# Kernel optimization log

Measured on AMD Instinct MI355X. Metric: run time of the kernel, lower is better.

Reference implementation:

```python
import itertools
import jax, jax.numpy as jnp
import numpy as np

# --- static configuration (matches init_kwargs) ---
B, O, V = 16, 24, 2            # batch, num_objects, num_total_variables
P0, P1, P2 = 32, 64, 64        # nullary/unary/binary predicate widths
R, C = 3, 16                   # len(arities)=3 ([0,1,2]), num_conjuncts
UI, BI = 1, 2                  # unary_index, binary_index in sorted arities [0,1,2]
NUM_IN = P0 + V * P1 + V * (V - 1) * P2  # 288

# permutation index tables (precomputed constants, as in build())
PERM_IDXS = np.array(list(itertools.permutations(range(O), V)))  # [P, V]
P = PERM_IDXS.shape[0]  # O*(O-1) = 552
_bin_idxs = np.stack(np.nonzero(1 - np.eye(V))).T.reshape(V, V - 1, 2)
_perm_bidxs = PERM_IDXS[:, _bin_idxs]                       # [P, V, V-1, 2]
_shift = (_perm_bidxs[..., 1] > _perm_bidxs[..., 0]).astype(int)
PERM_BIDXS = np.stack([_perm_bidxs[..., 0], _perm_bidxs[..., 1] - _shift], -1)  # [P,V,V-1,2]
BI0 = jnp.asarray(PERM_BIDXS[..., 0])
BI1 = jnp.asarray(PERM_BIDXS[..., 1])


def _probsum(x, axis):
    """Probabilistic OR reduction: 1 - prod(1 - x)."""
    return 1.0 - jnp.prod(1.0 - x, axis=axis)


def setup_inputs() -> dict:
    key = jax.random.key(0)
    k0, k1, k2, k3, k4 = jax.random.split(key, 5)
    return {
        "nullary": jax.random.uniform(k0, (B, P0), dtype=jnp.float32),
        "unary": jax.random.uniform(k1, (B, O, P1), dtype=jnp.float32),
        "binary": jax.random.uniform(k2, (B, O, O - 1, P2), dtype=jnp.float32),
        "and_kernel": 1.0 + 0.1 * jax.random.normal(k3, (R, C, NUM_IN, 3), dtype=jnp.float32),
        "or_kernel": 1.0 + 0.1 * jax.random.normal(k4, (R, C), dtype=jnp.float32),
        "temperature": jnp.ones((), dtype=jnp.float32),
    }


def reference(nullary, unary, binary, and_kernel, or_kernel, temperature):
    # --- compute_permutations ---
    perm_nullary = jnp.broadcast_to(nullary[:, None], (B, P, P0))       # [B,P,P0]
    perm_unary = unary[:, PERM_IDXS]                                    # [B,P,V,P1]
    perm_binary = binary[:, BI0, BI1]                                   # [B,P,V,V-1,P2]
    in_tensor = jnp.concatenate(
        [perm_nullary, perm_unary.reshape(B, P, -1), perm_binary.reshape(B, P, -1)], -1
    )  # [B, P, NUM_IN]

    # --- conjunct (AND) evaluation ---
    ak = jax.nn.softmax(and_kernel / temperature, axis=-1)              # [R,C,NUM_IN,3]
    x = in_tensor[:, :, None, None]                                     # [B,P,1,1,NUM_IN]
    conj_eval = x * ak[..., 0] + (1.0 - x) * ak[..., 1] + ak[..., 2]    # [B,P,R,C,NUM_IN]
    conjuncts = jnp.prod(conj_eval, axis=-1)                            # [B,P,R,C]

    # --- per-arity permutation reductions (OR over unbound variables) ---
    nullary_rules = _probsum(conjuncts[..., :UI, :], axis=1)            # [B,UI,C]
    unary_rules = conjuncts[..., UI:BI, :].reshape(B, O, P // O, BI - UI, C)
    unary_rules = _probsum(unary_rules, axis=2)                         # [B,O,BI-UI,C]
    binary_rules = conjuncts[..., BI:, :].reshape(
        B, O, O - 1, P // (O * (O - 1)), R - BI, C
    )
    binary_rules = _probsum(binary_rules, axis=3)                       # [B,O,O-1,R-BI,C]

    # --- disjunction (OR) over conjuncts ---
    ok = jax.nn.sigmoid(or_kernel / temperature)                        # [R,C]
    nullary_out = _probsum(nullary_rules * ok[:UI], -1)                 # [B,UI]
    unary_out = _probsum(unary_rules * ok[UI:BI], -1)                   # [B,O,BI-UI]
    binary_out = _probsum(binary_rules * ok[BI:], -1)                   # [B,O,O-1,R-BI]
    return nullary_out, unary_out, binary_out
```

## Files before the change

kernel.cpp:

```cpp
#include <hip/hip_runtime.h>
#include <math.h>


__device__ __forceinline__ float sigm(float x) { return 1.0f / (1.0f + expf(-x)); }

__global__ __launch_bounds__(256) void prep_kernel(const float* __restrict__ ak,
                                                   const float* __restrict__ temp,
                                                   float* __restrict__ dke) {
    int idx = blockIdx.x * 256 + threadIdx.x;
    if (idx >= 3 * 16 * 288) return;
    int i = idx % 288;
    int c = (idx / 288) % 16;
    int r = idx / (16 * 288);
    float invT = 1.0f / temp[0];
    const float* p = ak + (size_t)idx * 3;
    float a0 = p[0] * invT, a1 = p[1] * invT, a2 = p[2] * invT;
    float mx = fmaxf(a0, fmaxf(a1, a2));
    float e0 = expf(a0 - mx), e1 = expf(a1 - mx), e2 = expf(a2 - mx);
    float inv = 1.0f / (e0 + e1 + e2);
    float s0 = e0 * inv, s1 = e1 * inv, s2 = e2 * inv;
    int ch = i >> 2, lane = i & 3;
    float* q = dke + (((size_t)(ch * 16 + c) * 3 + r) * 8) + lane;
    q[0] = s0 - s1;
    q[4] = s1 + s2;
}

__global__ __launch_bounds__(256) void conj_part(const float* __restrict__ nullary,
                                                 const float* __restrict__ unary,
                                                 const float* __restrict__ binary,
                                                 const float* __restrict__ dke,
                                                 float* __restrict__ ws1) {
    __shared__ float xs[24 * 148];
    __shared__ float part[4][64][18];

    const int tid = threadIdx.x;
    const int blk = blockIdx.x;
    const int b = blk / 48;
    const int rem = blk % 48;
    const int a = rem >> 1;
    const int q = rem & 1;
    const int chbase = q * 36;

    for (int idx = tid; idx < 24 * 36; idx += 256) {
        int perm = idx / 36;
        int lc = idx % 36;
        int gc = chbase + lc;
        int je = perm < 23 ? perm : 22;
        int bb = je + (je >= a ? 1 : 0);
        int aadj = (a > bb) ? (a - 1) : a;
        const float* src;
        if (gc < 8)        src = nullary + b * 32 + gc * 4;
        else if (gc < 24)  src = unary + ((size_t)b * 24 + a) * 64 + (gc - 8) * 4;
        else if (gc < 40)  src = unary + ((size_t)b * 24 + bb) * 64 + (gc - 24) * 4;
        else if (gc < 56)  src = binary + (((size_t)b * 24 + a) * 23 + je) * 64 + (gc - 40) * 4;
        else               src = binary + (((size_t)b * 24 + bb) * 23 + aadj) * 64 + (gc - 56) * 4;
        float4 v = *(const float4*)src;
        *(float4*)&xs[perm * 148 + lc * 4] = v;
    }
    __syncthreads();

    const int iq = tid >> 6;
    const int pl = (tid >> 4) & 3;
    const int c  = tid & 15;

    float acc[6][3];
#pragma unroll
    for (int m = 0; m < 6; ++m)
#pragma unroll
        for (int r = 0; r < 3; ++r) acc[m][r] = 1.0f;

    const int lc0 = iq * 9;
#pragma unroll 3
    for (int lc = lc0; lc < lc0 + 9; ++lc) {
        float4 xv[6];
#pragma unroll
        for (int m = 0; m < 6; ++m)
            xv[m] = *(const float4*)&xs[(pl + 4 * m) * 148 + lc * 4];
        const float* kp = dke + (size_t)((chbase + lc) * 16 + c) * 24;
#pragma unroll
        for (int r = 0; r < 3; ++r) {
            float4 d = *(const float4*)(kp + r * 8);
            float4 e = *(const float4*)(kp + r * 8 + 4);
#pragma unroll
            for (int m = 0; m < 6; ++m) {
                float t0 = fmaf(xv[m].x, d.x, e.x);
                float t1 = fmaf(xv[m].y, d.y, e.y);
                float t2 = fmaf(xv[m].z, d.z, e.z);
                float t3 = fmaf(xv[m].w, d.w, e.w);
                acc[m][r] *= (t0 * t1) * (t2 * t3);
            }
        }
    }

    {
        float* p = part[iq][pl * 16 + c];
#pragma unroll
        for (int m = 0; m < 6; ++m)
#pragma unroll
            for (int r = 0; r < 3; ++r) p[m * 3 + r] = acc[m][r];
    }
    __syncthreads();

    if (iq == 0) {
        const int row = pl * 16 + c;
        float* dst = ws1 + (size_t)blk * 18 * 64;
#pragma unroll
        for (int m = 0; m < 6; ++m)
#pragma unroll
            for (int r = 0; r < 3; ++r)
                dst[(m * 3 + r) * 64 + row] =
                    part[0][row][m * 3 + r] * part[1][row][m * 3 + r]
                  * part[2][row][m * 3 + r] * part[3][row][m * 3 + r];
    }
}

__global__ __launch_bounds__(64) void combine_kernel(const float* __restrict__ ws1,
                                                     const float* __restrict__ orK,
                                                     const float* __restrict__ temp,
                                                     float* __restrict__ out,
                                                     float* __restrict__ ws0) {
    const int tid = threadIdx.x;
    const int b = blockIdx.x / 24;
    const int a = blockIdx.x % 24;
    const int pl = tid >> 4;
    const int c = tid & 15;

    const float* s0p = ws1 + ((size_t)(b * 48 + a * 2 + 0) * 18) * 64;
    const float* s1p = ws1 + ((size_t)(b * 48 + a * 2 + 1) * 18) * 64;

    float acc[6][3];
#pragma unroll
    for (int m = 0; m < 6; ++m)
#pragma unroll
        for (int r = 0; r < 3; ++r)
            acc[m][r] = s0p[(m * 3 + r) * 64 + tid] * s1p[(m * 3 + r) * 64 + tid];

    const float T = temp[0];
    const float ok2 = sigm(orK[32 + c] / T);

#pragma unroll
    for (int m = 0; m < 6; ++m) {
        int j = pl + 4 * m;
        float w = 1.0f - acc[m][2] * ok2;
#pragma unroll
        for (int off = 1; off < 16; off <<= 1) w *= __shfl_xor(w, off, 16);
        if (c == 0 && j < 23) out[400 + ((size_t)b * 24 + a) * 23 + j] = 1.0f - w;
    }

    float u1 = 1.0f, u0 = 1.0f;
#pragma unroll
    for (int m = 0; m < 6; ++m) {
        int j = pl + 4 * m;
        if (j < 23) {
            u1 *= (1.0f - acc[m][1]);
            u0 *= (1.0f - acc[m][0]);
        }
    }
    u1 *= __shfl_xor(u1, 16, 64);  u1 *= __shfl_xor(u1, 32, 64);
    u0 *= __shfl_xor(u0, 16, 64);  u0 *= __shfl_xor(u0, 32, 64);

    {
        float ok1 = sigm(orK[16 + c] / T);
        float w = 1.0f - (1.0f - u1) * ok1;
#pragma unroll
        for (int off = 1; off < 16; off <<= 1) w *= __shfl_xor(w, off, 16);
        if (tid == 0) out[16 + (size_t)b * 24 + a] = 1.0f - w;
    }
    if (pl == 0) ws0[((size_t)b * 24 + a) * 16 + c] = u0;
}

__global__ __launch_bounds__(256) void final_kernel(const float* __restrict__ ws0,
                                                    const float* __restrict__ orK,
                                                    const float* __restrict__ temp,
                                                    float* __restrict__ out) {
    int tid = threadIdx.x;
    int b = tid >> 4, c = tid & 15;
    float p = 1.0f;
#pragma unroll
    for (int a = 0; a < 24; ++a) p *= ws0[((size_t)b * 24 + a) * 16 + c];
    float T = temp[0];
    float ok0 = sigm(orK[c] / T);
    float w = 1.0f - (1.0f - p) * ok0;
#pragma unroll
    for (int off = 1; off < 16; off <<= 1) w *= __shfl_xor(w, off, 16);
    if (c == 0) out[b] = 1.0f - w;
}

extern "C" void kernel_launch(void* const* d_in, const int* in_sizes, int n_in,
                              void* d_out, int out_size, void* d_ws, size_t ws_size,
                              hipStream_t stream) {
    const float* nullary = (const float*)d_in[0];
    const float* unary   = (const float*)d_in[1];
    const float* binary  = (const float*)d_in[2];
    const float* ak      = (const float*)d_in[3];
    const float* orK     = (const float*)d_in[4];
    const float* temp    = (const float*)d_in[5];

    float* out = (float*)d_out;
    float* dke = (float*)d_ws;
    float* ws0 = dke + 27648;
    float* ws1 = ws0 + 6144;

    prep_kernel<<<54, 256, 0, stream>>>(ak, temp, dke);
    conj_part<<<768, 256, 0, stream>>>(nullary, unary, binary, dke, ws1);
    combine_kernel<<<384, 64, 0, stream>>>(ws1, orK, temp, out, ws0);
    final_kernel<<<1, 256, 0, stream>>>(ws0, orK, temp, out);
}
```

Measured before the change: 85.90 us.

## Fuse conjunct and combine kernels into one 512-thread block per (b,a)

```diff
diff --git a/kernel.cpp b/kernel.cpp
--- a/kernel.cpp
+++ b/kernel.cpp
@@ -1,6 +1,8 @@
 #include <hip/hip_runtime.h>
 #include <math.h>
 
+
+#define XST 290
 
 __device__ __forceinline__ float sigm(float x) { return 1.0f / (1.0f + expf(-x)); }
 
@@ -25,26 +27,24 @@
     q[4] = s1 + s2;
 }
 
-__global__ __launch_bounds__(256) void conj_part(const float* __restrict__ nullary,
-                                                 const float* __restrict__ unary,
-                                                 const float* __restrict__ binary,
-                                                 const float* __restrict__ dke,
-                                                 float* __restrict__ ws1) {
-    __shared__ float xs[24 * 148];
-    __shared__ float part[4][64][18];
+__global__ __launch_bounds__(512, 4) void mega_kernel(const float* __restrict__ nullary,
+                                                      const float* __restrict__ unary,
+                                                      const float* __restrict__ binary,
+                                                      const float* __restrict__ dke,
+                                                      const float* __restrict__ orK,
+                                                      const float* __restrict__ temp,
+                                                      float* __restrict__ out,
+                                                      float* __restrict__ ws0) {
+    __shared__ float xs[24 * XST];
+    __shared__ float part[7][64][18];
 
     const int tid = threadIdx.x;
-    const int blk = blockIdx.x;
-    const int b = blk / 48;
-    const int rem = blk % 48;
-    const int a = rem >> 1;
-    const int q = rem & 1;
-    const int chbase = q * 36;
-
-    for (int idx = tid; idx < 24 * 36; idx += 256) {
-        int perm = idx / 36;
-        int lc = idx % 36;
-        int gc = chbase + lc;
+    const int b = blockIdx.x / 24;
+    const int a = blockIdx.x % 24;
+
+    for (int idx = tid; idx < 24 * 72; idx += 512) {
+        int perm = idx / 72;
+        int gc = idx % 72;
         int je = perm < 23 ? perm : 22;
         int bb = je + (je >= a ? 1 : 0);
         int aadj = (a > bb) ? (a - 1) : a;
@@ -55,7 +55,7 @@
         else if (gc < 56)  src = binary + (((size_t)b * 24 + a) * 23 + je) * 64 + (gc - 40) * 4;
         else               src = binary + (((size_t)b * 24 + bb) * 23 + aadj) * 64 + (gc - 56) * 4;
         float4 v = *(const float4*)src;
-        *(float4*)&xs[perm * 148 + lc * 4] = v;
+        *(float4*)&xs[perm * XST + gc * 4] = v;
     }
     __syncthreads();
 
@@ -70,30 +70,67 @@
         for (int r = 0; r < 3; ++r) acc[m][r] = 1.0f;
 
     const int lc0 = iq * 9;
-#pragma unroll 3
-    for (int lc = lc0; lc < lc0 + 9; ++lc) {
+
+    float4 dcur[3], ecur[3];
+    {
+        const float* kp = dke + (size_t)(lc0 * 16 + c) * 24;
+#pragma unroll
+        for (int r = 0; r < 3; ++r) {
+            dcur[r] = *(const float4*)(kp + r * 8);
+            ecur[r] = *(const float4*)(kp + r * 8 + 4);
+        }
+    }
+
+#pragma unroll 2
+    for (int lc = lc0; lc < lc0 + 8; ++lc) {
+        float4 dnxt[3], enxt[3];
+        {
+            const float* kn = dke + (size_t)((lc + 1) * 16 + c) * 24;
+#pragma unroll
+            for (int r = 0; r < 3; ++r) {
+                dnxt[r] = *(const float4*)(kn + r * 8);
+                enxt[r] = *(const float4*)(kn + r * 8 + 4);
+            }
+        }
         float4 xv[6];
 #pragma unroll
         for (int m = 0; m < 6; ++m)
-            xv[m] = *(const float4*)&xs[(pl + 4 * m) * 148 + lc * 4];
-        const float* kp = dke + (size_t)((chbase + lc) * 16 + c) * 24;
+            xv[m] = *(const float4*)&xs[(pl + 4 * m) * XST + lc * 4];
 #pragma unroll
         for (int r = 0; r < 3; ++r) {
-            float4 d = *(const float4*)(kp + r * 8);
-            float4 e = *(const float4*)(kp + r * 8 + 4);
 #pragma unroll
             for (int m = 0; m < 6; ++m) {
-                float t0 = fmaf(xv[m].x, d.x, e.x);
-                float t1 = fmaf(xv[m].y, d.y, e.y);
-                float t2 = fmaf(xv[m].z, d.z, e.z);
-                float t3 = fmaf(xv[m].w, d.w, e.w);
+                float t0 = fmaf(xv[m].x, dcur[r].x, ecur[r].x);
+                float t1 = fmaf(xv[m].y, dcur[r].y, ecur[r].y);
+                float t2 = fmaf(xv[m].z, dcur[r].z, ecur[r].z);
+                float t3 = fmaf(xv[m].w, dcur[r].w, ecur[r].w);
                 acc[m][r] *= (t0 * t1) * (t2 * t3);
             }
         }
-    }
-
+#pragma unroll
+        for (int r = 0; r < 3; ++r) { dcur[r] = dnxt[r]; ecur[r] = enxt[r]; }
+    }
     {
-        float* p = part[iq][pl * 16 + c];
+        const int lc = lc0 + 8;
+        float4 xv[6];
+#pragma unroll
+        for (int m = 0; m < 6; ++m)
+            xv[m] = *(const float4*)&xs[(pl + 4 * m) * XST + lc * 4];
+#pragma unroll
+        for (int r = 0; r < 3; ++r) {
+#pragma unroll
+            for (int m = 0; m < 6; ++m) {
+                float t0 = fmaf(xv[m].x, dcur[r].x, ecur[r].x);
+                float t1 = fmaf(xv[m].y, dcur[r].y, ecur[r].y);
+                float t2 = fmaf(xv[m].z, dcur[r].z, ecur[r].z);
+                float t3 = fmaf(xv[m].w, dcur[r].w, ecur[r].w);
+                acc[m][r] *= (t0 * t1) * (t2 * t3);
+            }
+        }
+    }
+
+    if (iq >= 1) {
+        float* p = part[iq - 1][pl * 16 + c];
 #pragma unroll
         for (int m = 0; m < 6; ++m)
 #pragma unroll
@@ -103,70 +140,47 @@
 
     if (iq == 0) {
         const int row = pl * 16 + c;
-        float* dst = ws1 + (size_t)blk * 18 * 64;
-#pragma unroll
-        for (int m = 0; m < 6; ++m)
-#pragma unroll
-            for (int r = 0; r < 3; ++r)
-                dst[(m * 3 + r) * 64 + row] =
-                    part[0][row][m * 3 + r] * part[1][row][m * 3 + r]
-                  * part[2][row][m * 3 + r] * part[3][row][m * 3 + r];
-    }
-}
-
-__global__ __launch_bounds__(64) void combine_kernel(const float* __restrict__ ws1,
-                                                     const float* __restrict__ orK,
-                                                     const float* __restrict__ temp,
-                                                     float* __restrict__ out,
-                                                     float* __restrict__ ws0) {
-    const int tid = threadIdx.x;
-    const int b = blockIdx.x / 24;
-    const int a = blockIdx.x % 24;
-    const int pl = tid >> 4;
-    const int c = tid & 15;
-
-    const float* s0p = ws1 + ((size_t)(b * 48 + a * 2 + 0) * 18) * 64;
-    const float* s1p = ws1 + ((size_t)(b * 48 + a * 2 + 1) * 18) * 64;
-
-    float acc[6][3];
-#pragma unroll
-    for (int m = 0; m < 6; ++m)
-#pragma unroll
-        for (int r = 0; r < 3; ++r)
-            acc[m][r] = s0p[(m * 3 + r) * 64 + tid] * s1p[(m * 3 + r) * 64 + tid];
-
-    const float T = temp[0];
-    const float ok2 = sigm(orK[32 + c] / T);
-
-#pragma unroll
-    for (int m = 0; m < 6; ++m) {
-        int j = pl + 4 * m;
-        float w = 1.0f - acc[m][2] * ok2;
-#pragma unroll
-        for (int off = 1; off < 16; off <<= 1) w *= __shfl_xor(w, off, 16);
-        if (c == 0 && j < 23) out[400 + ((size_t)b * 24 + a) * 23 + j] = 1.0f - w;
-    }
-
-    float u1 = 1.0f, u0 = 1.0f;
-#pragma unroll
-    for (int m = 0; m < 6; ++m) {
-        int j = pl + 4 * m;
-        if (j < 23) {
-            u1 *= (1.0f - acc[m][1]);
-            u0 *= (1.0f - acc[m][0]);
-        }
-    }
-    u1 *= __shfl_xor(u1, 16, 64);  u1 *= __shfl_xor(u1, 32, 64);
-    u0 *= __shfl_xor(u0, 16, 64);  u0 *= __shfl_xor(u0, 32, 64);
-
-    {
-        float ok1 = sigm(orK[16 + c] / T);
-        float w = 1.0f - (1.0f - u1) * ok1;
-#pragma unroll
-        for (int off = 1; off < 16; off <<= 1) w *= __shfl_xor(w, off, 16);
-        if (tid == 0) out[16 + (size_t)b * 24 + a] = 1.0f - w;
-    }
-    if (pl == 0) ws0[((size_t)b * 24 + a) * 16 + c] = u0;
+#pragma unroll
+        for (int s = 0; s < 7; ++s)
+#pragma unroll
+            for (int m = 0; m < 6; ++m)
+#pragma unroll
+                for (int r = 0; r < 3; ++r)
+                    acc[m][r] *= part[s][row][m * 3 + r];
+
+        const float T = temp[0];
+        const float ok2 = sigm(orK[32 + c] / T);
+
+#pragma unroll
+        for (int m = 0; m < 6; ++m) {
+            int j = pl + 4 * m;
+            float w = 1.0f - acc[m][2] * ok2;
+#pragma unroll
+            for (int off = 1; off < 16; off <<= 1) w *= __shfl_xor(w, off, 16);
+            if (c == 0 && j < 23) out[400 + ((size_t)b * 24 + a) * 23 + j] = 1.0f - w;
+        }
+
+        float u1 = 1.0f, u0 = 1.0f;
+#pragma unroll
+        for (int m = 0; m < 6; ++m) {
+            int j = pl + 4 * m;
+            if (j < 23) {
+                u1 *= (1.0f - acc[m][1]);
+                u0 *= (1.0f - acc[m][0]);
+            }
+        }
+        u1 *= __shfl_xor(u1, 16, 64);  u1 *= __shfl_xor(u1, 32, 64);
+        u0 *= __shfl_xor(u0, 16, 64);  u0 *= __shfl_xor(u0, 32, 64);
+
+        {
+            float ok1 = sigm(orK[16 + c] / T);
+            float w = 1.0f - (1.0f - u1) * ok1;
+#pragma unroll
+            for (int off = 1; off < 16; off <<= 1) w *= __shfl_xor(w, off, 16);
+            if (tid == 0) out[16 + (size_t)b * 24 + a] = 1.0f - w;
+        }
+        if (pl == 0) ws0[((size_t)b * 24 + a) * 16 + c] = u0;
+    }
 }
 
 __global__ __launch_bounds__(256) void final_kernel(const float* __restrict__ ws0,
@@ -199,10 +213,8 @@
     float* out = (float*)d_out;
     float* dke = (float*)d_ws;
     float* ws0 = dke + 27648;
-    float* ws1 = ws0 + 6144;
 
     prep_kernel<<<54, 256, 0, stream>>>(ak, temp, dke);
-    conj_part<<<768, 256, 0, stream>>>(nullary, unary, binary, dke, ws1);
-    combine_kernel<<<384, 64, 0, stream>>>(ws1, orK, temp, out, ws0);
+    mega_kernel<<<16 * 24, 512, 0, stream>>>(nullary, unary, binary, dke, orK, temp, out, ws0);
     final_kernel<<<1, 256, 0, stream>>>(ws0, orK, temp, out);
 }
```

Measured after the change: 85.83 us. No clear change (-0.1%).

## Fuse conjunct evaluation and combine into one 1024-thread kernel per two objects

Applied to the files above, without the earlier changes.

```diff
diff --git a/kernel.cpp b/kernel.cpp
--- a/kernel.cpp
+++ b/kernel.cpp
@@ -1,6 +1,8 @@
 #include <hip/hip_runtime.h>
 #include <math.h>
 
+
+#define XST 290
 
 __device__ __forceinline__ float sigm(float x) { return 1.0f / (1.0f + expf(-x)); }
 
@@ -25,26 +27,26 @@
     q[4] = s1 + s2;
 }
 
-__global__ __launch_bounds__(256) void conj_part(const float* __restrict__ nullary,
-                                                 const float* __restrict__ unary,
-                                                 const float* __restrict__ binary,
-                                                 const float* __restrict__ dke,
-                                                 float* __restrict__ ws1) {
-    __shared__ float xs[24 * 148];
-    __shared__ float part[4][64][18];
+__global__ __launch_bounds__(1024, 4) void mega_kernel(const float* __restrict__ nullary,
+                                                       const float* __restrict__ unary,
+                                                       const float* __restrict__ binary,
+                                                       const float* __restrict__ dke,
+                                                       const float* __restrict__ orK,
+                                                       const float* __restrict__ temp,
+                                                       float* __restrict__ out,
+                                                       float* __restrict__ ws0) {
+    __shared__ float xs[2][24 * XST];
+    __shared__ float part[2][7][64][18];
 
     const int tid = threadIdx.x;
-    const int blk = blockIdx.x;
-    const int b = blk / 48;
-    const int rem = blk % 48;
-    const int a = rem >> 1;
-    const int q = rem & 1;
-    const int chbase = q * 36;
+    const int half = tid >> 9;
+    const int t9 = tid & 511;
+    const int b = blockIdx.x / 12;
+    const int a = (blockIdx.x % 12) * 2 + half;
 
-    for (int idx = tid; idx < 24 * 36; idx += 256) {
-        int perm = idx / 36;
-        int lc = idx % 36;
-        int gc = chbase + lc;
+    for (int idx = t9; idx < 24 * 72; idx += 512) {
+        int perm = idx / 72;
+        int gc = idx % 72;
         int je = perm < 23 ? perm : 22;
         int bb = je + (je >= a ? 1 : 0);
         int aadj = (a > bb) ? (a - 1) : a;
@@ -55,13 +57,13 @@
         else if (gc < 56)  src = binary + (((size_t)b * 24 + a) * 23 + je) * 64 + (gc - 40) * 4;
         else               src = binary + (((size_t)b * 24 + bb) * 23 + aadj) * 64 + (gc - 56) * 4;
         float4 v = *(const float4*)src;
-        *(float4*)&xs[perm * 148 + lc * 4] = v;
+        *(float4*)&xs[half][perm * XST + gc * 4] = v;
     }
     __syncthreads();
 
-    const int iq = tid >> 6;
-    const int pl = (tid >> 4) & 3;
-    const int c  = tid & 15;
+    const int iq = t9 >> 6;
+    const int pl = (t9 >> 4) & 3;
+    const int c  = t9 & 15;
 
     float acc[6][3];
 #pragma unroll
@@ -75,8 +77,8 @@
         float4 xv[6];
 #pragma unroll
         for (int m = 0; m < 6; ++m)
-            xv[m] = *(const float4*)&xs[(pl + 4 * m) * 148 + lc * 4];
-        const float* kp = dke + (size_t)((chbase + lc) * 16 + c) * 24;
+            xv[m] = *(const float4*)&xs[half][(pl + 4 * m) * XST + lc * 4];
+        const float* kp = dke + (size_t)(lc * 16 + c) * 24;
 #pragma unroll
         for (int r = 0; r < 3; ++r) {
             float4 d = *(const float4*)(kp + r * 8);
@@ -92,8 +94,8 @@
         }
     }
 
-    {
-        float* p = part[iq][pl * 16 + c];
+    if (iq >= 1) {
+        float* p = part[half][iq - 1][pl * 16 + c];
 #pragma unroll
         for (int m = 0; m < 6; ++m)
 #pragma unroll
@@ -103,70 +105,47 @@
 
     if (iq == 0) {
         const int row = pl * 16 + c;
-        float* dst = ws1 + (size_t)blk * 18 * 64;
 #pragma unroll
-        for (int m = 0; m < 6; ++m)
+        for (int s = 0; s < 7; ++s)
 #pragma unroll
-            for (int r = 0; r < 3; ++r)
-                dst[(m * 3 + r) * 64 + row] =
-                    part[0][row][m * 3 + r] * part[1][row][m * 3 + r]
-                  * part[2][row][m * 3 + r] * part[3][row][m * 3 + r];
-    }
-}
+            for (int m = 0; m < 6; ++m)
+#pragma unroll
+                for (int r = 0; r < 3; ++r)
+                    acc[m][r] *= part[half][s][row][m * 3 + r];
 
-__global__ __launch_bounds__(64) void combine_kernel(const float* __restrict__ ws1,
-                                                     const float* __restrict__ orK,
-                                                     const float* __restrict__ temp,
-                                                     float* __restrict__ out,
-                                                     float* __restrict__ ws0) {
-    const int tid = threadIdx.x;
-    const int b = blockIdx.x / 24;
-    const int a = blockIdx.x % 24;
-    const int pl = tid >> 4;
-    const int c = tid & 15;
-
-    const float* s0p = ws1 + ((size_t)(b * 48 + a * 2 + 0) * 18) * 64;
-    const float* s1p = ws1 + ((size_t)(b * 48 + a * 2 + 1) * 18) * 64;
-
-    float acc[6][3];
-#pragma unroll
-    for (int m = 0; m < 6; ++m)
-#pragma unroll
-        for (int r = 0; r < 3; ++r)
-            acc[m][r] = s0p[(m * 3 + r) * 64 + tid] * s1p[(m * 3 + r) * 64 + tid];
-
-    const float T = temp[0];
-    const float ok2 = sigm(orK[32 + c] / T);
+        const float T = temp[0];
+        const float ok2 = sigm(orK[32 + c] / T);
 
 #pragma unroll
-    for (int m = 0; m < 6; ++m) {
-        int j = pl + 4 * m;
-        float w = 1.0f - acc[m][2] * ok2;
+        for (int m = 0; m < 6; ++m) {
+            int j = pl + 4 * m;
+            float w = 1.0f - acc[m][2] * ok2;
 #pragma unroll
-        for (int off = 1; off < 16; off <<= 1) w *= __shfl_xor(w, off, 16);
-        if (c == 0 && j < 23) out[400 + ((size_t)b * 24 + a) * 23 + j] = 1.0f - w;
+            for (int off = 1; off < 16; off <<= 1) w *= __shfl_xor(w, off, 16);
+            if (c == 0 && j < 23) out[400 + ((size_t)b * 24 + a) * 23 + j] = 1.0f - w;
+        }
+
+        float u1 = 1.0f, u0 = 1.0f;
+#pragma unroll
+        for (int m = 0; m < 6; ++m) {
+            int j = pl + 4 * m;
+            if (j < 23) {
+                u1 *= (1.0f - acc[m][1]);
+                u0 *= (1.0f - acc[m][0]);
+            }
+        }
+        u1 *= __shfl_xor(u1, 16, 64);  u1 *= __shfl_xor(u1, 32, 64);
+        u0 *= __shfl_xor(u0, 16, 64);  u0 *= __shfl_xor(u0, 32, 64);
+
+        {
+            float ok1 = sigm(orK[16 + c] / T);
+            float w = 1.0f - (1.0f - u1) * ok1;
+#pragma unroll
+            for (int off = 1; off < 16; off <<= 1) w *= __shfl_xor(w, off, 16);
+            if (t9 == 0) out[16 + (size_t)b * 24 + a] = 1.0f - w;
+        }
+        if (pl == 0) ws0[((size_t)b * 24 + a) * 16 + c] = u0;
     }
-
-    float u1 = 1.0f, u0 = 1.0f;
-#pragma unroll
-    for (int m = 0; m < 6; ++m) {
-        int j = pl + 4 * m;
-        if (j < 23) {
-            u1 *= (1.0f - acc[m][1]);
-            u0 *= (1.0f - acc[m][0]);
-        }
-    }
-    u1 *= __shfl_xor(u1, 16, 64);  u1 *= __shfl_xor(u1, 32, 64);
-    u0 *= __shfl_xor(u0, 16, 64);  u0 *= __shfl_xor(u0, 32, 64);
-
-    {
-        float ok1 = sigm(orK[16 + c] / T);
-        float w = 1.0f - (1.0f - u1) * ok1;
-#pragma unroll
-        for (int off = 1; off < 16; off <<= 1) w *= __shfl_xor(w, off, 16);
-        if (tid == 0) out[16 + (size_t)b * 24 + a] = 1.0f - w;
-    }
-    if (pl == 0) ws0[((size_t)b * 24 + a) * 16 + c] = u0;
 }
 
 __global__ __launch_bounds__(256) void final_kernel(const float* __restrict__ ws0,
@@ -199,10 +178,8 @@
     float* out = (float*)d_out;
     float* dke = (float*)d_ws;
     float* ws0 = dke + 27648;
-    float* ws1 = ws0 + 6144;
 
     prep_kernel<<<54, 256, 0, stream>>>(ak, temp, dke);
-    conj_part<<<768, 256, 0, stream>>>(nullary, unary, binary, dke, ws1);
-    combine_kernel<<<384, 64, 0, stream>>>(ws1, orK, temp, out, ws0);
+    mega_kernel<<<16 * 12, 1024, 0, stream>>>(nullary, unary, binary, dke, orK, temp, out, ws0);
     final_kernel<<<1, 256, 0, stream>>>(ws0, orK, temp, out);
 }
```

After: 87.82 us. 2.2% more time.
